# Performance work log

Measured on AMD Instinct MI355X. Metric: run time of the kernel, lower is better.

## Reference

```python
import jax, jax.numpy as jnp
import numpy as np

NUM_CODEWORDS = 16384
EMBED_DIM = 4096      # == in_features (asserted in torch module)
OUT_FEATURES = 4096
N_TILES = 4
ROWS_PER_TILE = 1024  # N_TILES * ROWS_PER_TILE == OUT_FEATURES
B, S = 4, 2048


def setup_inputs() -> dict:
    key = jax.random.key(0)
    k1, k2, k3, k4, k5 = jax.random.split(key, 5)
    x = jax.random.normal(k1, (B, S, EMBED_DIM), dtype=jnp.float32)
    codewords = jax.random.normal(k2, (NUM_CODEWORDS, EMBED_DIM), dtype=jnp.float32) * 0.02
    indices = jax.random.randint(k3, (N_TILES, ROWS_PER_TILE), 0, NUM_CODEWORDS, dtype=jnp.int64)
    rotations = jax.random.normal(k4, (N_TILES, EMBED_DIM, EMBED_DIM), dtype=jnp.float32) / np.sqrt(EMBED_DIM)
    scales = jax.random.uniform(k5, (N_TILES,), dtype=jnp.float32)
    bias = jnp.zeros((OUT_FEATURES,), dtype=jnp.float32)
    return {"x": x, "codewords": codewords, "indices": indices,
            "rotations": rotations, "scales": scales, "bias": bias}


def _decode_weight(codewords, indices, rotations, scales):
    # gather: [T, R, D]
    decoded = codewords[indices]
    # per-tile rotation: [T, R, D] @ [T, D, D] -> [T, R, D]
    rotated = jnp.einsum('trd,tde->tre', decoded, rotations)
    scaled = rotated * scales[:, None, None]
    # concat tiles along rows -> [out_features, in_features]
    return scaled.reshape(-1, EMBED_DIM)


def reference(x, codewords, indices, rotations, scales, bias):
    weight = _decode_weight(codewords, indices, rotations, scales)  # [O, I]
    # F.linear: x @ weight.T + bias
    return jnp.einsum('bsi,oi->bso', x, weight) + bias
```

## Files before the change

kernel.cpp:

```cpp
#include <hip/hip_runtime.h>
#include <hip/hip_bf16.h>
#include <stdint.h>
#include <stddef.h>

#define DIM    4096
#define MROWS  8192
#define NCW    16384
#define NTILES 4
#define RPT    1024

#define BM 256
#define BN 256
#define BK 64
#define NT (DIM / BK)

typedef __attribute__((ext_vector_type(8))) short bf16x8;
typedef __attribute__((ext_vector_type(4))) float f32x4;

__device__ __forceinline__ uint16_t f2bf(float f) {
  union { float f; uint32_t u; } a; a.f = f;
  uint32_t u = a.u;
  u += 0x7fffu + ((u >> 16) & 1u);
  return (uint16_t)(u >> 16);
}

__device__ __forceinline__ void gl2lds16(const void* g, void* l) {
  __builtin_amdgcn_global_load_lds(
      (const __attribute__((address_space(1))) void*)g,
      (__attribute__((address_space(3))) void*)l, 16, 0, 0);
}

__device__ __forceinline__ bf16x8 lds_frag(const uint16_t* base, int r, int q) {
  int y = (r << 6) | (q << 4);
  y ^= ((y >> 7) & 7) << 4;
  return *(const bf16x8*)((const char*)base + y);
}

__global__ void detect_idx_kernel(const uint32_t* __restrict__ inds,
                                  int* __restrict__ flag) {
  __shared__ int bad;
  if (threadIdx.x == 0) bad = 0;
  __syncthreads();
  int viol = 0;
  for (int k = threadIdx.x; k < 2048; k += 256) {
    uint32_t lo = inds[2 * k];
    uint32_t hi = inds[2 * k + 1];
    if (hi != 0u || lo >= (uint32_t)NCW) viol = 1;
  }
  if (viol) atomicAdd(&bad, 1);
  __syncthreads();
  if (threadIdx.x == 0) flag[0] = (bad == 0) ? 1 : 0;
}

__global__ void cvt_x_kernel(const float* __restrict__ in,
                             uint16_t* __restrict__ out) {
  size_t i = ((size_t)blockIdx.x * 256 + threadIdx.x) * 8;
  float4 v0 = *(const float4*)(in + i);
  float4 v1 = *(const float4*)(in + i + 4);
  uint4 o;
  o.x = (uint32_t)f2bf(v0.x) | ((uint32_t)f2bf(v0.y) << 16);
  o.y = (uint32_t)f2bf(v0.z) | ((uint32_t)f2bf(v0.w) << 16);
  o.z = (uint32_t)f2bf(v1.x) | ((uint32_t)f2bf(v1.y) << 16);
  o.w = (uint32_t)f2bf(v1.z) | ((uint32_t)f2bf(v1.w) << 16);
  *(uint4*)(out + i) = o;
}

__global__ void gather_cw_kernel(const float* __restrict__ cw,
                                 const void* __restrict__ inds,
                                 const int* __restrict__ flag,
                                 uint16_t* __restrict__ out) {
  const int o = blockIdx.x;
  long long idx;
  if (flag[0]) idx = ((const long long*)inds)[o];
  else         idx = (long long)((const int*)inds)[o];
  const float* src = cw + (size_t)idx * DIM;
  uint16_t* dst = out + (size_t)o * DIM;
  for (int c = 0; c < 4; c++) {
    int e = c * 1024 + threadIdx.x * 4;
    float4 v = *(const float4*)(src + e);
    uint2 w;
    w.x = (uint32_t)f2bf(v.x) | ((uint32_t)f2bf(v.y) << 16);
    w.y = (uint32_t)f2bf(v.z) | ((uint32_t)f2bf(v.w) << 16);
    *(uint2*)(dst + e) = w;
  }
}

__global__ void rot_transpose_kernel(const float* __restrict__ R,
                                     uint16_t* __restrict__ Rt) {
  __shared__ float tile[32][33];
  const int t = blockIdx.z;
  const int e0 = blockIdx.x * 32;
  const int d0 = blockIdx.y * 32;
  const float* Rp = R + (size_t)t * DIM * DIM;
  uint16_t* Rtp = Rt + (size_t)t * DIM * DIM;
  for (int i = threadIdx.y; i < 32; i += 8)
    tile[i][threadIdx.x] = Rp[(size_t)(d0 + i) * DIM + (e0 + threadIdx.x)];
  __syncthreads();
  for (int i = threadIdx.y; i < 32; i += 8)
    Rtp[(size_t)(e0 + i) * DIM + (d0 + threadIdx.x)] = f2bf(tile[threadIdx.x][i]);
}

template <int MODE>
__global__ __launch_bounds__(512, 2)
void gemm256(const uint16_t* __restrict__ A,
             const uint16_t* __restrict__ B,
             const float* __restrict__ sv,
             void* __restrict__ Cout) {
  __shared__ __align__(16) uint16_t As[2][2][BM * 32];
  __shared__ __align__(16) uint16_t Bs[2][2][BN * 32];

  const int tid  = threadIdx.x;
  const int wave = tid >> 6;
  const int lane = tid & 63;
  const int quad = lane >> 4;
  const int lr   = lane & 15;
  const int wm   = (wave >> 2) * 128;
  const int wn   = (wave & 3) * 64;

  const int nwg = gridDim.x;
  const int bid = blockIdx.x;
  const int wg  = (bid & 7) * (nwg >> 3) + (bid >> 3);
  const int bx  = wg & 15;
  const int by  = wg >> 4;
  const int m0  = by * BM;
  const int n0  = bx * BN;

  const uint16_t* Bp = B;
  float scale = 1.0f;
  if (MODE == 0) {
    const int t = m0 >> 10;
    Bp = B + (size_t)t * DIM * DIM;
    scale = sv[t];
  }

  const int y0  = tid << 4;
  const int y1  = (512 + tid) << 4;
  const int gy0 = y0 ^ (((y0 >> 7) & 7) << 4);
  const int gy1 = y1 ^ (((y1 >> 7) & 7) << 4);
  const size_t ao0 = (size_t)(gy0 >> 6) * DIM + (size_t)((gy0 >> 4) & 3) * 8;
  const size_t ao1 = (size_t)(gy1 >> 6) * DIM + (size_t)((gy1 >> 4) & 3) * 8;
  const int ld0 = (wave * 64) * 8;
  const int ld1 = 4096 + (wave * 64) * 8;

  const uint16_t* Ag = A  + (size_t)m0 * DIM;
  const uint16_t* Bg = Bp + (size_t)n0 * DIM;

#define STG(gb, kc, lh)                          \
  do {                                           \
    gl2lds16((gb) + ao0 + (kc), (lh) + ld0);     \
    gl2lds16((gb) + ao1 + (kc), (lh) + ld1);     \
  } while (0)

  f32x4 acc[8][4];
#pragma unroll
  for (int i = 0; i < 8; i++)
#pragma unroll
    for (int j = 0; j < 4; j++) acc[i][j] = f32x4{0.f, 0.f, 0.f, 0.f};

  STG(Ag, 0,  As[0][0]);
  STG(Bg, 0,  Bs[0][0]);
  STG(Ag, 32, As[0][1]);
  STG(Bg, 32, Bs[0][1]);
  asm volatile("s_waitcnt vmcnt(4)" ::: "memory");
  __builtin_amdgcn_s_barrier();

  int cur = 0;
  bf16x8 b[4];

#define PHASE(KS, MH, STAGE_STMT, DO_VM)                                      \
  do {                                                                        \
    const uint16_t* Ab = As[cur][KS];                                         \
    bf16x8 a[4];                                                              \
    _Pragma("unroll")                                                         \
    for (int j = 0; j < 4; ++j)                                               \
      a[j] = lds_frag(Ab, wm + ((MH)*4 + j) * 16 + lr, quad);                 \
    if ((MH) == 0) {                                                          \
      const uint16_t* Bb = Bs[cur][KS];                                       \
      _Pragma("unroll")                                                       \
      for (int j = 0; j < 4; ++j)                                             \
        b[j] = lds_frag(Bb, wn + j * 16 + lr, quad);                          \
    }                                                                         \
    STAGE_STMT;                                                               \
    __builtin_amdgcn_s_barrier();                                             \
    asm volatile("s_waitcnt lgkmcnt(0)" ::: "memory");                        \
    __builtin_amdgcn_sched_barrier(0);                                        \
    __builtin_amdgcn_s_setprio(1);                                            \
    _Pragma("unroll")                                                         \
    for (int j = 0; j < 4; ++j)                                               \
      _Pragma("unroll")                                                       \
      for (int n = 0; n < 4; ++n)                                             \
        acc[(MH)*4 + j][n] = __builtin_amdgcn_mfma_f32_16x16x32_bf16(         \
            a[j], b[n], acc[(MH)*4 + j][n], 0, 0, 0);                         \
    __builtin_amdgcn_s_setprio(0);                                            \
    if (DO_VM) asm volatile("s_waitcnt vmcnt(4)" ::: "memory");               \
    __builtin_amdgcn_s_barrier();                                             \
  } while (0)

  for (int kt = 0; kt < NT; ++kt) {
    const int kn = (kt + 1 < NT) ? (kt + 1) * BK : kt * BK;
    PHASE(0, 0, STG(Ag, kn,      As[cur ^ 1][0]), 0);
    PHASE(0, 1, STG(Bg, kn,      Bs[cur ^ 1][0]), 1);
    PHASE(1, 0, STG(Ag, kn + 32, As[cur ^ 1][1]), 0);
    PHASE(1, 1, STG(Bg, kn + 32, Bs[cur ^ 1][1]), 1);
    cur ^= 1;
  }
  asm volatile("s_waitcnt vmcnt(0)" ::: "memory");

#undef PHASE
#undef STG

  if (MODE == 0) {
    uint16_t* C = (uint16_t*)Cout;
#pragma unroll
    for (int mi = 0; mi < 8; mi++)
#pragma unroll
      for (int ni = 0; ni < 4; ni++)
#pragma unroll
        for (int r = 0; r < 4; r++) {
          int row = m0 + wm + mi * 16 + quad * 4 + r;
          int col = n0 + wn + ni * 16 + lr;
          C[(size_t)row * DIM + col] = f2bf(acc[mi][ni][r] * scale);
        }
  } else {
    float* C = (float*)Cout;
#pragma unroll
    for (int mi = 0; mi < 8; mi++)
#pragma unroll
      for (int ni = 0; ni < 4; ni++)
#pragma unroll
        for (int r = 0; r < 4; r++) {
          int row = m0 + wm + mi * 16 + quad * 4 + r;
          int col = n0 + wn + ni * 16 + lr;
          C[(size_t)row * DIM + col] = acc[mi][ni][r] + sv[col];
        }
  }
}

extern "C" void kernel_launch(void* const* d_in, const int* in_sizes, int n_in,
                              void* d_out, int out_size, void* d_ws,
                              size_t ws_size, hipStream_t stream) {
  const float* x      = (const float*)d_in[0];
  const float* cw     = (const float*)d_in[1];
  const void*  inds   = d_in[2];
  const float* rot    = (const float*)d_in[3];
  const float* scales = (const float*)d_in[4];
  const float* bias   = (const float*)d_in[5];
  float* out = (float*)d_out;

  char* ws = (char*)d_ws;
  int*      flag = (int*)ws;
  uint16_t* Xb   = (uint16_t*)(ws + 256);
  uint16_t* Cgb  = (uint16_t*)(ws + 256 + (size_t)64  * 1024 * 1024);
  uint16_t* Rt   = (uint16_t*)(ws + 256 + (size_t)96  * 1024 * 1024);
  uint16_t* Wb   = (uint16_t*)(ws + 256 + (size_t)224 * 1024 * 1024);

  detect_idx_kernel<<<1, 256, 0, stream>>>((const uint32_t*)inds, flag);

  cvt_x_kernel<<<16384, 256, 0, stream>>>(x, Xb);

  gather_cw_kernel<<<DIM, 256, 0, stream>>>(cw, inds, flag, Cgb);

  rot_transpose_kernel<<<dim3(DIM / 32, DIM / 32, NTILES), dim3(32, 8), 0,
                         stream>>>(rot, Rt);

  gemm256<0><<<dim3((DIM / BN) * (DIM / BM)), 512, 0, stream>>>(
      Cgb, Rt, scales, (void*)Wb);

  gemm256<1><<<dim3((DIM / BN) * (MROWS / BM)), 512, 0, stream>>>(
      Xb, Wb, bias, (void*)out);
}
```

Before: 1.118 ms.

## Pipeline LDS fragment loads in GEMM and vectorize rotation transpose

The GEMM main loop now double-buffers A and B fragments in registers. The LDS reads for the next sub-phase are issued before the MFMAs of the current one, and the per-phase lgkmcnt(0) wait and double barrier are replaced by one barrier per phase with vmcnt(2) waits. This aims to hide LDS latency behind matrix math and cut synchronization overhead, at the cost of more live registers and a more delicate ordering of buffer reuse. Separately, the rotation transpose kernel moves to 64x64 tiles with float4 loads and packed 16-byte bf16 stores, reducing memory transactions in that preprocessing step.

```diff
diff --git a/kernel.cpp b/kernel.cpp
--- a/kernel.cpp
+++ b/kernel.cpp
@@ -87,17 +87,40 @@
 
 __global__ void rot_transpose_kernel(const float* __restrict__ R,
                                      uint16_t* __restrict__ Rt) {
-  __shared__ float tile[32][33];
+  __shared__ float tile[64][65];
   const int t = blockIdx.z;
-  const int e0 = blockIdx.x * 32;
-  const int d0 = blockIdx.y * 32;
+  const int e0 = blockIdx.x * 64;
+  const int d0 = blockIdx.y * 64;
   const float* Rp = R + (size_t)t * DIM * DIM;
   uint16_t* Rtp = Rt + (size_t)t * DIM * DIM;
-  for (int i = threadIdx.y; i < 32; i += 8)
-    tile[i][threadIdx.x] = Rp[(size_t)(d0 + i) * DIM + (e0 + threadIdx.x)];
+
+  const int tx = threadIdx.x & 15;
+  const int ty = threadIdx.x >> 4;
+#pragma unroll
+  for (int i = 0; i < 4; ++i) {
+    int d = ty + i * 16;
+    float4 v = *(const float4*)(Rp + (size_t)(d0 + d) * DIM + e0 + tx * 4);
+    tile[d][tx * 4 + 0] = v.x;
+    tile[d][tx * 4 + 1] = v.y;
+    tile[d][tx * 4 + 2] = v.z;
+    tile[d][tx * 4 + 3] = v.w;
+  }
   __syncthreads();
-  for (int i = threadIdx.y; i < 32; i += 8)
-    Rtp[(size_t)(e0 + i) * DIM + (d0 + threadIdx.x)] = f2bf(tile[threadIdx.x][i]);
+
+  const int g = threadIdx.x & 7;
+  const int e = threadIdx.x >> 3;
+#pragma unroll
+  for (int i = 0; i < 2; ++i) {
+    int ee = e + i * 32;
+    uint32_t w[4];
+#pragma unroll
+    for (int p = 0; p < 4; ++p) {
+      float lo = tile[g * 8 + 2 * p    ][ee];
+      float hi = tile[g * 8 + 2 * p + 1][ee];
+      w[p] = (uint32_t)f2bf(lo) | ((uint32_t)f2bf(hi) << 16);
+    }
+    *(uint4*)(Rtp + (size_t)(e0 + ee) * DIM + d0 + g * 8) = *(uint4*)w;
+  }
 }
 
 template <int MODE>
@@ -151,11 +174,41 @@
     gl2lds16((gb) + ao1 + (kc), (lh) + ld1);     \
   } while (0)
 
+#define LDA(dst, half, mh)                                       \
+  do {                                                           \
+    const uint16_t* _p = (half);                                 \
+    _Pragma("unroll")                                            \
+    for (int j = 0; j < 4; ++j)                                  \
+      dst[j] = lds_frag(_p, wm + ((mh) * 4 + j) * 16 + lr, quad);\
+  } while (0)
+
+#define LDB(dst, half)                                           \
+  do {                                                           \
+    const uint16_t* _p = (half);                                 \
+    _Pragma("unroll")                                            \
+    for (int j = 0; j < 4; ++j)                                  \
+      dst[j] = lds_frag(_p, wn + j * 16 + lr, quad);             \
+  } while (0)
+
+#define MFMA16(MH, AA, BB)                                            \
+  do {                                                                \
+    __builtin_amdgcn_s_setprio(1);                                    \
+    _Pragma("unroll")                                                 \
+    for (int j = 0; j < 4; ++j)                                       \
+      _Pragma("unroll")                                               \
+      for (int n = 0; n < 4; ++n)                                     \
+        acc[(MH) * 4 + j][n] = __builtin_amdgcn_mfma_f32_16x16x32_bf16(\
+            AA[j], BB[n], acc[(MH) * 4 + j][n], 0, 0, 0);             \
+    __builtin_amdgcn_s_setprio(0);                                    \
+  } while (0)
+
   f32x4 acc[8][4];
 #pragma unroll
   for (int i = 0; i < 8; i++)
 #pragma unroll
     for (int j = 0; j < 4; j++) acc[i][j] = f32x4{0.f, 0.f, 0.f, 0.f};
+
+  bf16x8 a0[4], a1[4], b0[4], b1[4];
 
   STG(Ag, 0,  As[0][0]);
   STG(Bg, 0,  Bs[0][0]);
@@ -163,50 +216,44 @@
   STG(Bg, 32, Bs[0][1]);
   asm volatile("s_waitcnt vmcnt(4)" ::: "memory");
   __builtin_amdgcn_s_barrier();
+  LDA(a0, As[0][0], 0);
+  LDB(b0, Bs[0][0]);
 
   int cur = 0;
-  bf16x8 b[4];
-
-#define PHASE(KS, MH, STAGE_STMT, DO_VM)                                      \
-  do {                                                                        \
-    const uint16_t* Ab = As[cur][KS];                                         \
-    bf16x8 a[4];                                                              \
-    _Pragma("unroll")                                                         \
-    for (int j = 0; j < 4; ++j)                                               \
-      a[j] = lds_frag(Ab, wm + ((MH)*4 + j) * 16 + lr, quad);                 \
-    if ((MH) == 0) {                                                          \
-      const uint16_t* Bb = Bs[cur][KS];                                       \
-      _Pragma("unroll")                                                       \
-      for (int j = 0; j < 4; ++j)                                             \
-        b[j] = lds_frag(Bb, wn + j * 16 + lr, quad);                          \
-    }                                                                         \
-    STAGE_STMT;                                                               \
-    __builtin_amdgcn_s_barrier();                                             \
-    asm volatile("s_waitcnt lgkmcnt(0)" ::: "memory");                        \
-    __builtin_amdgcn_sched_barrier(0);                                        \
-    __builtin_amdgcn_s_setprio(1);                                            \
-    _Pragma("unroll")                                                         \
-    for (int j = 0; j < 4; ++j)                                               \
-      _Pragma("unroll")                                                       \
-      for (int n = 0; n < 4; ++n)                                             \
-        acc[(MH)*4 + j][n] = __builtin_amdgcn_mfma_f32_16x16x32_bf16(         \
-            a[j], b[n], acc[(MH)*4 + j][n], 0, 0, 0);                         \
-    __builtin_amdgcn_s_setprio(0);                                            \
-    if (DO_VM) asm volatile("s_waitcnt vmcnt(4)" ::: "memory");               \
-    __builtin_amdgcn_s_barrier();                                             \
-  } while (0)
-
   for (int kt = 0; kt < NT; ++kt) {
     const int kn = (kt + 1 < NT) ? (kt + 1) * BK : kt * BK;
-    PHASE(0, 0, STG(Ag, kn,      As[cur ^ 1][0]), 0);
-    PHASE(0, 1, STG(Bg, kn,      Bs[cur ^ 1][0]), 1);
-    PHASE(1, 0, STG(Ag, kn + 32, As[cur ^ 1][1]), 0);
-    PHASE(1, 1, STG(Bg, kn + 32, Bs[cur ^ 1][1]), 1);
+
+    __builtin_amdgcn_s_barrier();
+    LDA(a1, As[cur][0], 1);
+    STG(Ag, kn, As[cur ^ 1][0]);
+    MFMA16(0, a0, b0);
+    asm volatile("s_waitcnt vmcnt(2)" ::: "memory");
+
+    __builtin_amdgcn_s_barrier();
+    LDA(a0, As[cur][1], 0);
+    LDB(b1, Bs[cur][1]);
+    STG(Bg, kn, Bs[cur ^ 1][0]);
+    MFMA16(1, a1, b0);
+
+    __builtin_amdgcn_s_barrier();
+    LDA(a1, As[cur][1], 1);
+    STG(Ag, kn + 32, As[cur ^ 1][1]);
+    MFMA16(0, a0, b1);
+    asm volatile("s_waitcnt vmcnt(2)" ::: "memory");
+
+    __builtin_amdgcn_s_barrier();
+    LDA(a0, As[cur ^ 1][0], 0);
+    LDB(b0, Bs[cur ^ 1][0]);
+    STG(Bg, kn + 32, Bs[cur ^ 1][1]);
+    MFMA16(1, a1, b1);
+
     cur ^= 1;
   }
   asm volatile("s_waitcnt vmcnt(0)" ::: "memory");
 
-#undef PHASE
+#undef MFMA16
+#undef LDB
+#undef LDA
 #undef STG
 
   if (MODE == 0) {
@@ -260,8 +307,8 @@
 
   gather_cw_kernel<<<DIM, 256, 0, stream>>>(cw, inds, flag, Cgb);
 
-  rot_transpose_kernel<<<dim3(DIM / 32, DIM / 32, NTILES), dim3(32, 8), 0,
-                         stream>>>(rot, Rt);
+  rot_transpose_kernel<<<dim3(DIM / 64, DIM / 64, NTILES), 256, 0, stream>>>(
+      rot, Rt);
 
   gemm256<0><<<dim3((DIM / BN) * (DIM / BM)), 512, 0, stream>>>(
       Cgb, Rt, scales, (void*)Wb);
```

After: 1.011 ms. 1.11x faster.
